# Kernel tuning notes

Measured on AMD Instinct MI355X. Metric: run time of the kernel, lower is better.

The kernel has to match this reference:

```python
import jax, jax.numpy as jnp
import numpy as np

B, N, C, H, W = 16, 8, 3, 64, 96
PRED_BITS = 2
CONV_CH, FC, FMAP_H, FMAP_W = 16, 100, 16, 24


def _conv(x, Wc, bc):
    # x: [n, cin, 64, 96] -> [n, 16, 16, 24]; kernel 8x8, stride 4, pad 2
    y = jax.lax.conv_general_dilated(x, Wc, (4, 4), [(2, 2), (2, 2)],
                                     dimension_numbers=('NCHW', 'OIHW', 'NCHW'))
    return y + bc[None, :, None, None]


def _encoder(x, Wc, bc, W2, b2, W3, b3):
    h1 = jax.nn.relu(_conv(x, Wc, bc)).reshape(x.shape[0], -1)  # [n, 6144]
    h2 = jax.nn.relu(h1 @ W2 + b2)
    return h2 @ W3 + b3  # [n, PRED_BITS]


def _gumbel_softmax(logits, g, temp):
    return jax.nn.softmax((logits + g) / temp, axis=-1)


def setup_inputs() -> dict:
    key = jax.random.key(0)
    ks = jax.random.split(key, 16)
    rn = lambda k, s, sc=1.0: jax.random.normal(k, s, jnp.float32) * sc
    gum = lambda k, s: -jnp.log(-jnp.log(jax.random.uniform(k, s, jnp.float32, 1e-6, 1.0 - 1e-6)))
    inp = {
        'state': rn(ks[0], (B, N, C, H, W)),
        'state_next': rn(ks[1], (B, N, C, H, W)),
        'state_tilda': rn(ks[2], (B, N, C, H, W)),
        'n_obj': jax.random.randint(ks[3], (B,), 1, N + 1),
        'temp': jnp.asarray(1.0, jnp.float32),
        'g_unary': gum(ks[4], (3, B * N, PRED_BITS)),
        'g_binary': gum(ks[5], (3, B * N * N, PRED_BITS)),
        'Wc_u': rn(ks[6], (CONV_CH, C, 8, 8), 0.05),
        'bc_u': jnp.zeros((CONV_CH,), jnp.float32),
        'W2_u': rn(ks[7], (CONV_CH * FMAP_H * FMAP_W, FC), 0.02),
        'b2_u': jnp.zeros((FC,), jnp.float32),
        'W3_u': rn(ks[8], (FC, PRED_BITS), 0.1),
        'b3_u': jnp.zeros((PRED_BITS,), jnp.float32),
        'Wc_b': rn(ks[9], (CONV_CH, 2 * C, 8, 8), 0.05),
        'bc_b': jnp.zeros((CONV_CH,), jnp.float32),
        'W2_b': rn(ks[10], (CONV_CH * FMAP_H * FMAP_W, FC), 0.02),
        'b2_b': jnp.zeros((FC,), jnp.float32),
        'W3_b': rn(ks[11], (FC, PRED_BITS), 0.1),
        'b3_b': jnp.zeros((PRED_BITS,), jnp.float32),
    }
    return inp


def reference(state, state_next, state_tilda, n_obj, temp, g_unary, g_binary,
              Wc_u, bc_u, W2_u, b2_u, W3_u, b3_u,
              Wc_b, bc_b, W2_b, b2_b, W3_b, b3_b):
    # cartesian-product pair gather (padded to N_max^2 per sample)
    ii = jnp.arange(N * N) // N
    jj = jnp.arange(N * N) % N

    def pairs(s):  # [B,N,C,H,W] -> [B*N*N, 2C, H, W]
        return jnp.concatenate([s[:, ii], s[:, jj]], axis=2).reshape(B * N * N, 2 * C, H, W)

    def bin_pred(s, g):
        logits = _encoder(pairs(s), Wc_b, bc_b, W2_b, b2_b, W3_b, b3_b)
        return _gumbel_softmax(logits, g, temp).reshape(B, N * N, PRED_BITS)

    def un_pred(s, g):
        logits = _encoder(s.reshape(B * N, C, H, W), Wc_u, bc_u, W2_u, b2_u, W3_u, b3_u)
        return _gumbel_softmax(logits, g, temp).reshape(B, N, PRED_BITS)

    bp = bin_pred(state, g_binary[0])
    bp_n = bin_pred(state_next, g_binary[1])
    bp_t = bin_pred(state_tilda, g_binary[2])
    up = un_pred(state, g_unary[0])
    up_n = un_pred(state_next, g_unary[1])
    up_t = un_pred(state_tilda, g_unary[2])

    # compact the valid n^2 pairs to the front (matches torch padded scatter layout)
    n = n_obj[:, None]                      # [B,1]
    p = jnp.arange(N * N)[None, :]          # [1,N^2]
    ns = jnp.maximum(n, 1)
    k = (p // ns) * N + (p % ns)            # padded index of compact position p
    valid_b = (p < n * n)[:, :, None]
    kidx = jnp.clip(k, 0, N * N - 1)[:, :, None]

    def compact(x):
        return jnp.take_along_axis(x, kidx, axis=1) * valid_b

    valid_u = (jnp.arange(N)[None, :] < n)[:, :, None]

    return (compact(bp), compact(bp_n), compact(bp_t),
            up * valid_u, up_n * valid_u, up_t * valid_u)
```

## Files before the change

kernel.cpp:

```cpp
#include <hip/hip_runtime.h>
#include <hip/hip_bf16.h>


typedef __attribute__((ext_vector_type(8))) short bf16x8;
typedef __attribute__((ext_vector_type(4))) float f32x4;

__device__ inline unsigned short bf16u(float x) {
    __hip_bfloat16 h = __float2bfloat16(x);
    return __builtin_bit_cast(unsigned short, h);
}

__device__ inline unsigned pair_relu(unsigned f, unsigned s) {
    float lo = __builtin_bit_cast(float, f << 16) + __builtin_bit_cast(float, s << 16);
    float hi = __builtin_bit_cast(float, f & 0xffff0000u) + __builtin_bit_cast(float, s & 0xffff0000u);
    lo = lo > 0.f ? lo : 0.f;
    hi = hi > 0.f ? hi : 0.f;
    return (unsigned)bf16u(lo) | ((unsigned)bf16u(hi) << 16);
}

#define CL_STRIDE 106
#define CL_CH (36 * CL_STRIDE)
__global__ __launch_bounds__(256) void conv_prep_kernel(
    const float* __restrict__ s0, const float* __restrict__ s1, const float* __restrict__ s2,
    const float* __restrict__ Wcu, const float* __restrict__ Wcb,
    const float* __restrict__ bcu, const float* __restrict__ bcb,
    const float* __restrict__ W2b, const float* __restrict__ W2u,
    unsigned short* __restrict__ Au, unsigned short* __restrict__ yfb,
    unsigned short* __restrict__ ysb,
    unsigned short* __restrict__ Btb, unsigned short* __restrict__ Btu)
{
    __shared__ __align__(16) unsigned short sh[3 * CL_CH];
    const int bx  = blockIdx.x;
    const int tid = threadIdx.x;

    if (bx >= 768) {
        const int bx2 = bx - 768;
        const int arr = bx2 / 48;
        const int k0 = (bx2 % 48) * 128;
        const float* W2 = arr ? W2u : W2b;
        unsigned short* Bt = arr ? Btu : Btb;
#pragma unroll
        for (int p = 0; p < 2; ++p) {
            const int kk0 = p * 64;
            __syncthreads();
            for (int t = tid; t < 64 * 128; t += 256) {
                int kk = t >> 7, f = t & 127;
                float v = (f < 100) ? W2[(long)(k0 + kk0 + kk) * 100 + f] : 0.f;
                sh[kk * 130 + f] = bf16u(v);
            }
            __syncthreads();
            for (int t = tid; t < 64 * 128; t += 256) {
                int f = t >> 6, kk = t & 63;
                Bt[(long)f * 6144 + k0 + kk0 + kk] = sh[kk * 130 + f];
            }
        }
        return;
    }

    const int si  = bx >> 8;
    const int rem = bx & 255;
    const int img = rem >> 1;
    const int h   = rem & 1;
    const float* simg = (si == 0 ? s0 : (si == 1 ? s1 : s2)) + (long)img * 18432;

    const int lane = tid & 63;
    const int w    = tid >> 6;
    const int quad = lane >> 4;
    const int lcol = lane & 15;

    {
        unsigned* d = (unsigned*)sh;
        const float4* Wu4 = (const float4*)Wcu;
        for (int l4 = tid; l4 < 768; l4 += 256) {
            int l = l4 * 4, ch = l / 192, e = l % 192;
            int g = (e >> 5) * 3;
            int bi = ((g * 64 + ((e >> 3) & 3) * 16 + ch) * 8 + (e & 7)) >> 1;
            float4 v = Wu4[l4];
            d[bi]     = (unsigned)bf16u(v.x) | ((unsigned)bf16u(v.y) << 16);
            d[bi + 1] = (unsigned)bf16u(v.z) | ((unsigned)bf16u(v.w) << 16);
        }
        const float4* Wb4 = (const float4*)Wcb;
        for (int l4 = tid; l4 < 1536; l4 += 256) {
            int l = l4 * 4, ch = l / 384, r = l % 384;
            int nt = (r < 192) ? 1 : 2, e = r % 192;
            int g = (e >> 5) * 3 + nt;
            int bi = ((g * 64 + ((e >> 3) & 3) * 16 + ch) * 8 + (e & 7)) >> 1;
            float4 v = Wb4[l4];
            d[bi]     = (unsigned)bf16u(v.x) | ((unsigned)bf16u(v.y) << 16);
            d[bi + 1] = (unsigned)bf16u(v.z) | ((unsigned)bf16u(v.w) << 16);
        }
    }
    __syncthreads();

    bf16x8 bw[6][3];
#pragma unroll
    for (int t6 = 0; t6 < 6; ++t6)
#pragma unroll
        for (int nt = 0; nt < 3; ++nt)
            bw[t6][nt] = *(const bf16x8*)(sh + ((t6 * 3 + nt) * 64 + lane) * 8);
    __syncthreads();

    for (int t = tid; t < (3 * CL_CH) / 2; t += 256)
        ((unsigned*)sh)[t] = 0u;
    __syncthreads();

    const int y0 = h * 32;
    for (int t = tid; t < 3 * 36 * 24; t += 256) {
        int c = t / 864, rq = t % 864, r = rq / 24, q = rq % 24;
        int iy = y0 + r - 2;
        if (iy >= 0 && iy < 64) {
            float4 v = *((const float4*)(simg + c * 6144 + iy * 96) + q);
            unsigned lo = (unsigned)bf16u(v.x) | ((unsigned)bf16u(v.y) << 16);
            unsigned hi = (unsigned)bf16u(v.z) | ((unsigned)bf16u(v.w) << 16);
            unsigned* dst = (unsigned*)(sh + c * CL_CH + r * CL_STRIDE + q * 4 + 4);
            dst[0] = lo; dst[1] = hi;
        }
    }
    __syncthreads();

    const float bu = bcu[lcol];
    const float bb = bcb[lcol];
    const long im = (long)si * 128 + img;
    unsigned short* Aur = Au + im * 6144;
    unsigned short* yfr = yfb + im * 6144;
    unsigned short* ysr = ysb + im * 6144;

#pragma unroll
    for (int mi = 0; mi < 3; ++mi) {
        const int mt = w * 3 + mi;
        const int p  = mt * 16 + lcol;
        const int oyl = p / 24, ox = p % 24;
        f32x4 a0 = {0.f, 0.f, 0.f, 0.f}, a1 = a0, a2 = a0;
#pragma unroll
        for (int t6 = 0; t6 < 6; ++t6) {
            int g  = t6 * 4 + quad;
            int c  = g >> 3, ky = g & 7;
            const unsigned* lp = (const unsigned*)(sh + c * CL_CH + (oyl * 4 + ky) * CL_STRIDE + ox * 4 + 2);
            bf16x8 afr;
            unsigned* ap = (unsigned*)&afr;
            ap[0] = lp[0]; ap[1] = lp[1]; ap[2] = lp[2]; ap[3] = lp[3];
            a0 = __builtin_amdgcn_mfma_f32_16x16x32_bf16(afr, bw[t6][0], a0, 0, 0, 0);
            a1 = __builtin_amdgcn_mfma_f32_16x16x32_bf16(afr, bw[t6][1], a1, 0, 0, 0);
            a2 = __builtin_amdgcn_mfma_f32_16x16x32_bf16(afr, bw[t6][2], a2, 0, 0, 0);
        }
        const int base = h * 192 + mt * 16 + quad * 4;
        ushort4 ou, of, os;
        {
            float u0 = a0[0] + bu, u1 = a0[1] + bu, u2 = a0[2] + bu, u3 = a0[3] + bu;
            ou.x = bf16u(u0 > 0.f ? u0 : 0.f);
            ou.y = bf16u(u1 > 0.f ? u1 : 0.f);
            ou.z = bf16u(u2 > 0.f ? u2 : 0.f);
            ou.w = bf16u(u3 > 0.f ? u3 : 0.f);
            of.x = bf16u(a1[0] + bb); of.y = bf16u(a1[1] + bb);
            of.z = bf16u(a1[2] + bb); of.w = bf16u(a1[3] + bb);
            os.x = bf16u(a2[0]); os.y = bf16u(a2[1]);
            os.z = bf16u(a2[2]); os.w = bf16u(a2[3]);
        }
        *(ushort4*)(Aur + lcol * 384 + base) = ou;
        *(ushort4*)(yfr + lcol * 384 + base) = of;
        *(ushort4*)(ysr + lcol * 384 + base) = os;
    }
}

__global__ __launch_bounds__(256) void gemm_kernel(
    const unsigned short* __restrict__ yfb, const unsigned short* __restrict__ ysb,
    const unsigned short* __restrict__ Au,
    const unsigned short* __restrict__ Btb, const unsigned short* __restrict__ Btu,
    float* __restrict__ partial)
{
    const int tid = threadIdx.x;
    const int mt = blockIdx.x % 54;
    const int kc = blockIdx.x / 54;

    __shared__ __align__(16) unsigned short lsA[64 * 72];
    __shared__ __align__(16) unsigned short lsB[128 * 72];

    const int lane = tid & 63;
    const int w  = tid >> 6;
    const int wr = w & 1;
    const int wc = w >> 1;
    const int quad = lane >> 4;
    const int lcol = lane & 15;

    f32x4 acc[2][4];
#pragma unroll
    for (int i = 0; i < 2; ++i)
#pragma unroll
        for (int j = 0; j < 4; ++j) acc[i][j] = (f32x4){0.f, 0.f, 0.f, 0.f};

    const int ra = tid >> 2, qa = tid & 3;
    const bool fused = (mt < 48);
    const unsigned short *pf, *ps = nullptr;
    if (fused) {
        int g = mt * 64 + ra;
        int si = g >> 10, gs = g & 1023;
        int b = gs >> 6, i = (gs >> 3) & 7, j = gs & 7;
        pf = yfb + (long)(si * 128 + b * 8 + i) * 6144;
        ps = ysb + (long)(si * 128 + b * 8 + j) * 6144;
    } else {
        pf = Au + (long)((mt - 48) * 64 + ra) * 6144;
    }
    const unsigned short* Bt = fused ? Btb : Btu;
    const int rb = tid >> 1, hb = tid & 1;
    const long brow = (long)rb * 6144;
    const int kbase0 = kc * 768;

    for (int it = 0; it < 12; ++it) {
        const int kb = kbase0 + it * 64;
        const uint4* gb = (const uint4*)(Bt + brow + kb + hb * 32);
        uint4 b0 = gb[0], b1 = gb[1], b2 = gb[2], b3 = gb[3];
        const uint4* gf = (const uint4*)(pf + kb + qa * 16);
        uint4 f0 = gf[0], f1 = gf[1];
        if (fused) {
            const uint4* gs2 = (const uint4*)(ps + kb + qa * 16);
            uint4 s0 = gs2[0], s1 = gs2[1];
            f0.x = pair_relu(f0.x, s0.x); f0.y = pair_relu(f0.y, s0.y);
            f0.z = pair_relu(f0.z, s0.z); f0.w = pair_relu(f0.w, s0.w);
            f1.x = pair_relu(f1.x, s1.x); f1.y = pair_relu(f1.y, s1.y);
            f1.z = pair_relu(f1.z, s1.z); f1.w = pair_relu(f1.w, s1.w);
        }
        uint4* da = (uint4*)(lsA + ra * 72 + qa * 16);
        uint4* db = (uint4*)(lsB + rb * 72 + hb * 32);
        da[0] = f0; da[1] = f1;
        db[0] = b0; db[1] = b1; db[2] = b2; db[3] = b3;
        __syncthreads();
#pragma unroll
        for (int ks = 0; ks < 2; ++ks) {
            bf16x8 af[2], bfr[4];
#pragma unroll
            for (int t = 0; t < 2; ++t)
                af[t] = *(const bf16x8*)(lsA + (wr * 32 + t * 16 + lcol) * 72 + ks * 32 + quad * 8);
#pragma unroll
            for (int t = 0; t < 4; ++t)
                bfr[t] = *(const bf16x8*)(lsB + (wc * 64 + t * 16 + lcol) * 72 + ks * 32 + quad * 8);
#pragma unroll
            for (int i = 0; i < 2; ++i)
#pragma unroll
                for (int j = 0; j < 4; ++j)
                    acc[i][j] = __builtin_amdgcn_mfma_f32_16x16x32_bf16(af[i], bfr[j], acc[i][j], 0, 0, 0);
        }
        __syncthreads();
    }

    float* out = partial + (long)(kc * 54 + mt) * 8192;
#pragma unroll
    for (int i = 0; i < 2; ++i)
#pragma unroll
        for (int j = 0; j < 4; ++j)
#pragma unroll
            for (int reg = 0; reg < 4; ++reg) {
                int rr = wr * 32 + i * 16 + quad * 4 + reg;
                int cc = wc * 64 + j * 16 + lcol;
                out[rr * 128 + cc] = acc[i][j][reg];
            }
}

__global__ __launch_bounds__(256) void head_kernel(
    const float* __restrict__ partial,
    const float* __restrict__ b2b, const float* __restrict__ b2u,
    const float* __restrict__ W3b, const float* __restrict__ b3b,
    const float* __restrict__ W3u, const float* __restrict__ b3u,
    const float* __restrict__ gb, const float* __restrict__ gu,
    const int* __restrict__ nobj, const float* __restrict__ temp_p,
    float* __restrict__ out)
{
    const int tid = threadIdx.x;
    const int dp = blockIdx.x * 16 + (tid >> 4);
    const int c = tid & 15;
    const bool un = dp >= 3072;

    int srcrow, validf;
    long gidx, oidx;
    if (!un) {
        int si = dp / 1024, rem = dp % 1024;
        int b = rem >> 6, p = rem & 63;
        int n = nobj[b];
        int ns = n > 0 ? n : 1;
        int k = (p / ns) * 8 + (p % ns);
        validf = p < n * n;
        int kk = k < 63 ? k : 63;
        srcrow = si * 1024 + b * 64 + kk;
        gidx = (long)srcrow * 2;
        oidx = (long)si * 2048 + (b * 64 + p) * 2;
    } else {
        int r = dp - 3072;
        int si = r / 128, q = r % 128;
        int b = q >> 3, i = q & 7;
        srcrow = 3072 + r;
        validf = i < nobj[b];
        gidx = (long)si * 256 + q * 2;
        oidx = 6144 + (long)si * 256 + q * 2;
    }

    const float* b2 = un ? b2u : b2b;
    const float* W3 = un ? W3u : W3b;
    const int mt = srcrow >> 6, rr = srcrow & 63;
    float l0 = 0.f, l1 = 0.f;
    for (int f = c; f < 100; f += 16) {
        float s = b2[f];
#pragma unroll
        for (int kc = 0; kc < 8; ++kc)
            s += partial[((long)(kc * 54 + mt) * 64 + rr) * 128 + f];
        float hv = s > 0.f ? s : 0.f;
        l0 = fmaf(hv, W3[f * 2],     l0);
        l1 = fmaf(hv, W3[f * 2 + 1], l1);
    }
#pragma unroll
    for (int off = 8; off >= 1; off >>= 1) {
        l0 += __shfl_xor(l0, off);
        l1 += __shfl_xor(l1, off);
    }
    if (c == 0) {
        const float* b3 = un ? b3u : b3b;
        const float* g = (un ? gu : gb) + gidx;
        float d = ((l0 + b3[0] + g[0]) - (l1 + b3[1] + g[1])) / temp_p[0];
        float p0 = 1.f / (1.f + expf(-d));
        out[oidx]     = validf ? p0 : 0.f;
        out[oidx + 1] = validf ? 1.f - p0 : 0.f;
    }
}

static const size_t YFB_OFF  = 0;
static const size_t YSB_OFF  = 4718592;
static const size_t AU_OFF   = 9437184;
static const size_t BTB_OFF  = 14155776;
static const size_t BTU_OFF  = 15728640;
static const size_t PART_OFF = 17301504;

extern "C" void kernel_launch(void* const* d_in, const int* in_sizes, int n_in,
                              void* d_out, int out_size, void* d_ws, size_t ws_size,
                              hipStream_t stream) {
    const float* state   = (const float*)d_in[0];
    const float* state_n = (const float*)d_in[1];
    const float* state_t = (const float*)d_in[2];
    const int*   n_obj   = (const int*)  d_in[3];
    const float* temp    = (const float*)d_in[4];
    const float* g_un    = (const float*)d_in[5];
    const float* g_bin   = (const float*)d_in[6];
    const float* Wc_u    = (const float*)d_in[7];
    const float* bc_u    = (const float*)d_in[8];
    const float* W2_u    = (const float*)d_in[9];
    const float* b2_u    = (const float*)d_in[10];
    const float* W3_u    = (const float*)d_in[11];
    const float* b3_u    = (const float*)d_in[12];
    const float* Wc_b    = (const float*)d_in[13];
    const float* bc_b    = (const float*)d_in[14];
    const float* W2_b    = (const float*)d_in[15];
    const float* b2_b    = (const float*)d_in[16];
    const float* W3_b    = (const float*)d_in[17];
    const float* b3_b    = (const float*)d_in[18];

    char* ws = (char*)d_ws;
    unsigned short* yfb  = (unsigned short*)(ws + YFB_OFF);
    unsigned short* ysb  = (unsigned short*)(ws + YSB_OFF);
    unsigned short* Au   = (unsigned short*)(ws + AU_OFF);
    unsigned short* Btb  = (unsigned short*)(ws + BTB_OFF);
    unsigned short* Btu  = (unsigned short*)(ws + BTU_OFF);
    float*          prt  = (float*)(ws + PART_OFF);
    float*          out  = (float*)d_out;

    hipLaunchKernelGGL(conv_prep_kernel, dim3(864), dim3(256), 0, stream,
                       state, state_n, state_t, Wc_u, Wc_b, bc_u, bc_b, W2_b, W2_u,
                       Au, yfb, ysb, Btb, Btu);
    hipLaunchKernelGGL(gemm_kernel, dim3(432), dim3(256), 0, stream,
                       yfb, ysb, Au, Btb, Btu, prt);
    hipLaunchKernelGGL(head_kernel, dim3(216), dim3(256), 0, stream,
                       prt, b2_b, b2_u, W3_b, b3_b, W3_u, b3_u,
                       g_bin, g_un, n_obj, temp, out);
}
```

Baseline: 156.3 us.

## Switch pipeline to fp16, stage conv outputs in LDS, halve partial-sum storage

Converts all intermediate activations and weights from bf16 to fp16 and uses the fp16 MFMA instructions. The pairwise add+ReLU becomes a packed 8-wide fp16 vector add and max instead of per-element unpack and repack through float. Conv outputs are now staged in shared memory and written out as coalesced 16-byte stores rather than scattered 8-byte stores. GEMM split-K partials are stored as fp16, which halves that traffic but risks overflow or precision loss in the partial sums.

```diff
diff --git a/kernel.cpp b/kernel.cpp
--- a/kernel.cpp
+++ b/kernel.cpp
@@ -1,21 +1,22 @@
 #include <hip/hip_runtime.h>
-#include <hip/hip_bf16.h>
-
-
-typedef __attribute__((ext_vector_type(8))) short bf16x8;
+#include <hip/hip_fp16.h>
+
+
+typedef __attribute__((ext_vector_type(8))) _Float16 f16x8;
 typedef __attribute__((ext_vector_type(4))) float f32x4;
 
-__device__ inline unsigned short bf16u(float x) {
-    __hip_bfloat16 h = __float2bfloat16(x);
+__device__ inline unsigned short h16u(float x) {
+    __half h = __float2half(x);
     return __builtin_bit_cast(unsigned short, h);
 }
 
-__device__ inline unsigned pair_relu(unsigned f, unsigned s) {
-    float lo = __builtin_bit_cast(float, f << 16) + __builtin_bit_cast(float, s << 16);
-    float hi = __builtin_bit_cast(float, f & 0xffff0000u) + __builtin_bit_cast(float, s & 0xffff0000u);
-    lo = lo > 0.f ? lo : 0.f;
-    hi = hi > 0.f ? hi : 0.f;
-    return (unsigned)bf16u(lo) | ((unsigned)bf16u(hi) << 16);
+__device__ inline uint4 pair_relu4(uint4 f, uint4 s) {
+    f16x8 a = __builtin_bit_cast(f16x8, f);
+    f16x8 b = __builtin_bit_cast(f16x8, s);
+    const f16x8 z = {0, 0, 0, 0, 0, 0, 0, 0};
+    f16x8 r = a + b;
+    r = __builtin_elementwise_max(r, z);
+    return __builtin_bit_cast(uint4, r);
 }
 
 #define CL_STRIDE 106
@@ -46,7 +47,7 @@
             for (int t = tid; t < 64 * 128; t += 256) {
                 int kk = t >> 7, f = t & 127;
                 float v = (f < 100) ? W2[(long)(k0 + kk0 + kk) * 100 + f] : 0.f;
-                sh[kk * 130 + f] = bf16u(v);
+                sh[kk * 130 + f] = h16u(v);
             }
             __syncthreads();
             for (int t = tid; t < 64 * 128; t += 256) {
@@ -76,8 +77,8 @@
             int g = (e >> 5) * 3;
             int bi = ((g * 64 + ((e >> 3) & 3) * 16 + ch) * 8 + (e & 7)) >> 1;
             float4 v = Wu4[l4];
-            d[bi]     = (unsigned)bf16u(v.x) | ((unsigned)bf16u(v.y) << 16);
-            d[bi + 1] = (unsigned)bf16u(v.z) | ((unsigned)bf16u(v.w) << 16);
+            d[bi]     = (unsigned)h16u(v.x) | ((unsigned)h16u(v.y) << 16);
+            d[bi + 1] = (unsigned)h16u(v.z) | ((unsigned)h16u(v.w) << 16);
         }
         const float4* Wb4 = (const float4*)Wcb;
         for (int l4 = tid; l4 < 1536; l4 += 256) {
@@ -86,18 +87,18 @@
             int g = (e >> 5) * 3 + nt;
             int bi = ((g * 64 + ((e >> 3) & 3) * 16 + ch) * 8 + (e & 7)) >> 1;
             float4 v = Wb4[l4];
-            d[bi]     = (unsigned)bf16u(v.x) | ((unsigned)bf16u(v.y) << 16);
-            d[bi + 1] = (unsigned)bf16u(v.z) | ((unsigned)bf16u(v.w) << 16);
-        }
-    }
-    __syncthreads();
-
-    bf16x8 bw[6][3];
+            d[bi]     = (unsigned)h16u(v.x) | ((unsigned)h16u(v.y) << 16);
+            d[bi + 1] = (unsigned)h16u(v.z) | ((unsigned)h16u(v.w) << 16);
+        }
+    }
+    __syncthreads();
+
+    f16x8 bw[6][3];
 #pragma unroll
     for (int t6 = 0; t6 < 6; ++t6)
 #pragma unroll
         for (int nt = 0; nt < 3; ++nt)
-            bw[t6][nt] = *(const bf16x8*)(sh + ((t6 * 3 + nt) * 64 + lane) * 8);
+            bw[t6][nt] = *(const f16x8*)(sh + ((t6 * 3 + nt) * 64 + lane) * 8);
     __syncthreads();
 
     for (int t = tid; t < (3 * CL_CH) / 2; t += 256)
@@ -110,8 +111,8 @@
         int iy = y0 + r - 2;
         if (iy >= 0 && iy < 64) {
             float4 v = *((const float4*)(simg + c * 6144 + iy * 96) + q);
-            unsigned lo = (unsigned)bf16u(v.x) | ((unsigned)bf16u(v.y) << 16);
-            unsigned hi = (unsigned)bf16u(v.z) | ((unsigned)bf16u(v.w) << 16);
+            unsigned lo = (unsigned)h16u(v.x) | ((unsigned)h16u(v.y) << 16);
+            unsigned hi = (unsigned)h16u(v.z) | ((unsigned)h16u(v.w) << 16);
             unsigned* dst = (unsigned*)(sh + c * CL_CH + r * CL_STRIDE + q * 4 + 4);
             dst[0] = lo; dst[1] = hi;
         }
@@ -120,45 +121,57 @@
 
     const float bu = bcu[lcol];
     const float bb = bcb[lcol];
-    const long im = (long)si * 128 + img;
-    unsigned short* Aur = Au + im * 6144;
-    unsigned short* yfr = yfb + im * 6144;
-    unsigned short* ysr = ysb + im * 6144;
+
+    f32x4 accs[3][3];
+#pragma unroll
+    for (int mi = 0; mi < 3; ++mi)
+#pragma unroll
+        for (int nt = 0; nt < 3; ++nt) accs[mi][nt] = (f32x4){0.f, 0.f, 0.f, 0.f};
 
 #pragma unroll
     for (int mi = 0; mi < 3; ++mi) {
         const int mt = w * 3 + mi;
         const int p  = mt * 16 + lcol;
         const int oyl = p / 24, ox = p % 24;
-        f32x4 a0 = {0.f, 0.f, 0.f, 0.f}, a1 = a0, a2 = a0;
 #pragma unroll
         for (int t6 = 0; t6 < 6; ++t6) {
             int g  = t6 * 4 + quad;
             int c  = g >> 3, ky = g & 7;
             const unsigned* lp = (const unsigned*)(sh + c * CL_CH + (oyl * 4 + ky) * CL_STRIDE + ox * 4 + 2);
-            bf16x8 afr;
+            f16x8 afr;
             unsigned* ap = (unsigned*)&afr;
             ap[0] = lp[0]; ap[1] = lp[1]; ap[2] = lp[2]; ap[3] = lp[3];
-            a0 = __builtin_amdgcn_mfma_f32_16x16x32_bf16(afr, bw[t6][0], a0, 0, 0, 0);
-            a1 = __builtin_amdgcn_mfma_f32_16x16x32_bf16(afr, bw[t6][1], a1, 0, 0, 0);
-            a2 = __builtin_amdgcn_mfma_f32_16x16x32_bf16(afr, bw[t6][2], a2, 0, 0, 0);
-        }
-        const int base = h * 192 + mt * 16 + quad * 4;
-        ushort4 ou, of, os;
-        {
-            float u0 = a0[0] + bu, u1 = a0[1] + bu, u2 = a0[2] + bu, u3 = a0[3] + bu;
-            ou.x = bf16u(u0 > 0.f ? u0 : 0.f);
-            ou.y = bf16u(u1 > 0.f ? u1 : 0.f);
-            ou.z = bf16u(u2 > 0.f ? u2 : 0.f);
-            ou.w = bf16u(u3 > 0.f ? u3 : 0.f);
-            of.x = bf16u(a1[0] + bb); of.y = bf16u(a1[1] + bb);
-            of.z = bf16u(a1[2] + bb); of.w = bf16u(a1[3] + bb);
-            os.x = bf16u(a2[0]); os.y = bf16u(a2[1]);
-            os.z = bf16u(a2[2]); os.w = bf16u(a2[3]);
-        }
-        *(ushort4*)(Aur + lcol * 384 + base) = ou;
-        *(ushort4*)(yfr + lcol * 384 + base) = of;
-        *(ushort4*)(ysr + lcol * 384 + base) = os;
+            accs[mi][0] = __builtin_amdgcn_mfma_f32_16x16x32_f16(afr, bw[t6][0], accs[mi][0], 0, 0, 0);
+            accs[mi][1] = __builtin_amdgcn_mfma_f32_16x16x32_f16(afr, bw[t6][1], accs[mi][1], 0, 0, 0);
+            accs[mi][2] = __builtin_amdgcn_mfma_f32_16x16x32_f16(afr, bw[t6][2], accs[mi][2], 0, 0, 0);
+        }
+    }
+    __syncthreads();
+
+#pragma unroll
+    for (int mi = 0; mi < 3; ++mi) {
+        const int base = (w * 3 + mi) * 16 + quad * 4;
+#pragma unroll
+        for (int nt = 0; nt < 3; ++nt) {
+            ushort4 o;
+#pragma unroll
+            for (int reg = 0; reg < 4; ++reg) {
+                float v = accs[mi][nt][reg];
+                if (nt == 0) { v += bu; v = v > 0.f ? v : 0.f; }
+                else if (nt == 1) v += bb;
+                ((unsigned short*)&o)[reg] = h16u(v);
+            }
+            *(ushort4*)(sh + (nt * 16 + lcol) * 200 + base) = o;
+        }
+    }
+    __syncthreads();
+
+    const long im = (long)si * 128 + img;
+    unsigned short* outp[3] = { Au + im * 6144, yfb + im * 6144, ysb + im * 6144 };
+    for (int t = tid; t < 1152; t += 256) {
+        int nt = t / 384, r = t % 384, ch = r / 24, q = r % 24;
+        uint4 v = *(const uint4*)(sh + (nt * 16 + ch) * 200 + q * 8);
+        *(uint4*)(outp[nt] + ch * 384 + h * 192 + q * 8) = v;
     }
 }
 
@@ -166,7 +179,7 @@
     const unsigned short* __restrict__ yfb, const unsigned short* __restrict__ ysb,
     const unsigned short* __restrict__ Au,
     const unsigned short* __restrict__ Btb, const unsigned short* __restrict__ Btu,
-    float* __restrict__ partial)
+    __half* __restrict__ partial)
 {
     const int tid = threadIdx.x;
     const int mt = blockIdx.x % 54;
@@ -213,11 +226,8 @@
         uint4 f0 = gf[0], f1 = gf[1];
         if (fused) {
             const uint4* gs2 = (const uint4*)(ps + kb + qa * 16);
-            uint4 s0 = gs2[0], s1 = gs2[1];
-            f0.x = pair_relu(f0.x, s0.x); f0.y = pair_relu(f0.y, s0.y);
-            f0.z = pair_relu(f0.z, s0.z); f0.w = pair_relu(f0.w, s0.w);
-            f1.x = pair_relu(f1.x, s1.x); f1.y = pair_relu(f1.y, s1.y);
-            f1.z = pair_relu(f1.z, s1.z); f1.w = pair_relu(f1.w, s1.w);
+            f0 = pair_relu4(f0, gs2[0]);
+            f1 = pair_relu4(f1, gs2[1]);
         }
         uint4* da = (uint4*)(lsA + ra * 72 + qa * 16);
         uint4* db = (uint4*)(lsB + rb * 72 + hb * 32);
@@ -226,23 +236,23 @@
         __syncthreads();
 #pragma unroll
         for (int ks = 0; ks < 2; ++ks) {
-            bf16x8 af[2], bfr[4];
+            f16x8 af[2], bfr[4];
 #pragma unroll
             for (int t = 0; t < 2; ++t)
-                af[t] = *(const bf16x8*)(lsA + (wr * 32 + t * 16 + lcol) * 72 + ks * 32 + quad * 8);
+                af[t] = *(const f16x8*)(lsA + (wr * 32 + t * 16 + lcol) * 72 + ks * 32 + quad * 8);
 #pragma unroll
             for (int t = 0; t < 4; ++t)
-                bfr[t] = *(const bf16x8*)(lsB + (wc * 64 + t * 16 + lcol) * 72 + ks * 32 + quad * 8);
+                bfr[t] = *(const f16x8*)(lsB + (wc * 64 + t * 16 + lcol) * 72 + ks * 32 + quad * 8);
 #pragma unroll
             for (int i = 0; i < 2; ++i)
 #pragma unroll
                 for (int j = 0; j < 4; ++j)
-                    acc[i][j] = __builtin_amdgcn_mfma_f32_16x16x32_bf16(af[i], bfr[j], acc[i][j], 0, 0, 0);
+                    acc[i][j] = __builtin_amdgcn_mfma_f32_16x16x32_f16(af[i], bfr[j], acc[i][j], 0, 0, 0);
         }
         __syncthreads();
     }
 
-    float* out = partial + (long)(kc * 54 + mt) * 8192;
+    __half* out = partial + (long)(kc * 54 + mt) * 8192;
 #pragma unroll
     for (int i = 0; i < 2; ++i)
 #pragma unroll
@@ -251,12 +261,12 @@
             for (int reg = 0; reg < 4; ++reg) {
                 int rr = wr * 32 + i * 16 + quad * 4 + reg;
                 int cc = wc * 64 + j * 16 + lcol;
-                out[rr * 128 + cc] = acc[i][j][reg];
+                out[rr * 128 + cc] = __float2half(acc[i][j][reg]);
             }
 }
 
 __global__ __launch_bounds__(256) void head_kernel(
-    const float* __restrict__ partial,
+    const __half* __restrict__ partial,
     const float* __restrict__ b2b, const float* __restrict__ b2u,
     const float* __restrict__ W3b, const float* __restrict__ b3b,
     const float* __restrict__ W3u, const float* __restrict__ b3u,
@@ -300,7 +310,7 @@
         float s = b2[f];
 #pragma unroll
         for (int kc = 0; kc < 8; ++kc)
-            s += partial[((long)(kc * 54 + mt) * 64 + rr) * 128 + f];
+            s += __half2float(partial[((long)(kc * 54 + mt) * 64 + rr) * 128 + f]);
         float hv = s > 0.f ? s : 0.f;
         l0 = fmaf(hv, W3[f * 2],     l0);
         l1 = fmaf(hv, W3[f * 2 + 1], l1);
@@ -356,7 +366,7 @@
     unsigned short* Au   = (unsigned short*)(ws + AU_OFF);
     unsigned short* Btb  = (unsigned short*)(ws + BTB_OFF);
     unsigned short* Btu  = (unsigned short*)(ws + BTU_OFF);
-    float*          prt  = (float*)(ws + PART_OFF);
+    __half*         prt  = (__half*)(ws + PART_OFF);
     float*          out  = (float*)d_out;
 
     hipLaunchKernelGGL(conv_prep_kernel, dim3(864), dim3(256), 0, stream,
```

After: 150.4 us. -3.7%, faster.
